# Kernel tuning notes

Hardware: AMD Instinct MI355X
Metric: run time of the kernel (lower is better)

Reference implementation:

```python
import jax, jax.numpy as jnp
import numpy as np

B, IN_DIM, UNITS = 16384, 3072, 3072  # batch, input_dim=3*unit1, units=3*unit2


def setup_inputs() -> dict:
    key = jax.random.key(0)
    k1, k2, k3 = jax.random.split(key, 3)
    inputs = jax.random.normal(k1, (B, IN_DIM), dtype=jnp.float32)
    # original init: uniform [0, 0.01) for w, zeros for b (gpe_bias = [0, 0])
    w = jax.random.uniform(k2, (IN_DIM, UNITS), dtype=jnp.float32, minval=0.0, maxval=0.01)
    b = jnp.zeros((UNITS,), dtype=jnp.float32)
    # per-unit binary diagonal mask, stored as [units, input_dim]
    mask = jax.random.randint(k3, (UNITS, IN_DIM), 0, 2, dtype=jnp.int32)
    return {"inputs": inputs, "w": w, "b": b, "mask": mask}


def reference(inputs, w, b, mask):
    # Original: p = transpose(s @ inputs^T, [2,0,1]) -> [batch, units, input_dim]
    #           f = diag_part(p @ w) + b            -> [batch, units]
    # Since s[u] = diag(mask[u]), this is exactly:
    #   f[b,u] = sum_i inputs[b,i] * mask[u,i] * w[i,u] + b[u]
    # i.e. a single masked GEMM with effective weight w * mask^T.
    w_eff = w * mask.T.astype(w.dtype)  # [input_dim, units]
    return inputs @ w_eff + b
```

## Files before the change

kernel.cpp:

```cpp
#include <hip/hip_runtime.h>

#define BATCH 16384
#define KDIM  3072
#define NDIM  3072

typedef __bf16 bf16;
typedef bf16  bf16x8  __attribute__((ext_vector_type(8)));
typedef float f32x4   __attribute__((ext_vector_type(4)));

__device__ __forceinline__ void g2l16(const bf16* g, bf16* l) {
    __builtin_amdgcn_global_load_lds(
        (__attribute__((address_space(1))) unsigned int*)g,
        (__attribute__((address_space(3))) unsigned int*)l,
        16, 0, 0);
}

__global__ __launch_bounds__(256) void cvt_a_kernel(const float* __restrict__ in,
                                                    bf16* __restrict__ out) {
    const long idx = (long)blockIdx.x * 256 + threadIdx.x;
    const float4* in4 = (const float4*)in;
    float4 a = in4[idx * 2];
    float4 b = in4[idx * 2 + 1];
    bf16x8 o;
    o[0] = (bf16)a.x; o[1] = (bf16)a.y; o[2] = (bf16)a.z; o[3] = (bf16)a.w;
    o[4] = (bf16)b.x; o[5] = (bf16)b.y; o[6] = (bf16)b.z; o[7] = (bf16)b.w;
    ((bf16x8*)out)[idx] = o;
}

__global__ __launch_bounds__(256) void weff_kernel(const float* __restrict__ w,
                                                   const int* __restrict__ mask,
                                                   bf16* __restrict__ wt) {
    __shared__ float tile[32][33];
    const int i0 = blockIdx.x * 32;
    const int u0 = blockIdx.y * 32;
    const int tx = threadIdx.x, ty = threadIdx.y;
#pragma unroll
    for (int r = 0; r < 4; r++)
        tile[ty + 8 * r][tx] = w[(long)(i0 + ty + 8 * r) * NDIM + u0 + tx];
    __syncthreads();
#pragma unroll
    for (int r = 0; r < 4; r++) {
        int u = u0 + ty + 8 * r;
        int i = i0 + tx;
        float v = tile[tx][ty + 8 * r] * (float)mask[(long)u * KDIM + i];
        wt[(long)u * KDIM + i] = (bf16)v;
    }
}

__global__ __launch_bounds__(512, 2) void gemm_kernel(const bf16* __restrict__ A,
                                                      const bf16* __restrict__ Bt,
                                                      const float* __restrict__ bias,
                                                      float* __restrict__ C) {
    __shared__ __align__(16) bf16 lds[2 * 32768];

    const int tid  = threadIdx.x;
    const int lane = tid & 63;
    const int wv   = tid >> 6;
    const int l15  = lane & 15;
    const int l4   = lane >> 4;
    const int sx   = l15 & 7;
    const int wm   = (wv >> 2) * 64;
    const int wn   = (wv & 3) * 32;

    const int lid = blockIdx.y * gridDim.x + blockIdx.x;
    const int sid = (lid & 7) * 96 + (lid >> 3);
    const long m0 = (long)(sid / 12) * 256;
    const long n0 = (long)(sid % 12) * 256;

    const int srow = tid >> 3;
    const int gsc  = (tid & 7) ^ (srow & 7);
    const bf16* gAb = A  + (m0 + srow) * (long)KDIM + gsc * 8;
    const bf16* gBb = Bt + (n0 + srow) * (long)KDIM + gsc * 8;

#define STAGE_A(Q, KT, H) do {                                                  \
    const bf16* g_ = gAb + (long)((H) * 128) * KDIM + (long)(KT) * 64;          \
    bf16* d_ = &lds[(Q) * 32768 + (H) * 8192 + tid * 8];                        \
    g2l16(g_, d_);                                                              \
    g2l16(g_ + (long)64 * KDIM, d_ + 4096);                                     \
} while (0)
#define STAGE_B(Q, KT, H) do {                                                  \
    const bf16* g_ = gBb + (long)((H) * 128) * KDIM + (long)(KT) * 64;          \
    bf16* d_ = &lds[(Q) * 32768 + 16384 + (H) * 8192 + tid * 8];                \
    g2l16(g_, d_);                                                              \
    g2l16(g_ + (long)64 * KDIM, d_ + 4096);                                     \
} while (0)

    const int aRow = (wm + l15) * 64;
    const int bRow = (wn + l15) * 64;
    const int cc0  = (l4 ^ sx) * 8;
    const int cc1  = cc0 ^ 32;

    bf16x8 aF[4][2];
    bf16x8 bF[4][2];
    f32x4  acc[8][4] = {};

#define RDA(BP, MH)                                                             \
    _Pragma("unroll") for (int f_ = 0; f_ < 4; ++f_) {                          \
        aF[f_][0] = *(const bf16x8*)((BP) + (MH) * 8192 + aRow + f_ * 1024 + cc0); \
        aF[f_][1] = *(const bf16x8*)((BP) + (MH) * 8192 + aRow + f_ * 1024 + cc1); \
    }
#define RDB(BP, NH)                                                             \
    _Pragma("unroll") for (int n_ = 0; n_ < 2; ++n_) {                          \
        bF[(NH) * 2 + n_][0] = *(const bf16x8*)((BP) + 16384 + (NH) * 8192 + bRow + n_ * 1024 + cc0); \
        bF[(NH) * 2 + n_][1] = *(const bf16x8*)((BP) + 16384 + (NH) * 8192 + bRow + n_ * 1024 + cc1); \
    }
#define MMQ(MH, NH)                                                             \
    _Pragma("unroll") for (int ks_ = 0; ks_ < 2; ++ks_)                         \
    _Pragma("unroll") for (int f_ = 0; f_ < 4; ++f_)                            \
    _Pragma("unroll") for (int n_ = 0; n_ < 2; ++n_)                            \
        acc[(MH) * 4 + f_][(NH) * 2 + n_] = __builtin_amdgcn_mfma_f32_16x16x32_bf16( \
            aF[f_][ks_], bF[(NH) * 2 + n_][ks_], acc[(MH) * 4 + f_][(NH) * 2 + n_], 0, 0, 0)

#define PHASE(P, MH, NH, READS, STAGE_STMT, DOVM) do {                          \
    const bf16* bp_ = &lds[(P) * 32768];                                        \
    READS;                                                                      \
    STAGE_STMT;                                                                 \
    __builtin_amdgcn_s_setprio(1);                                              \
    MMQ(MH, NH);                                                                \
    __builtin_amdgcn_s_setprio(0);                                              \
    __builtin_amdgcn_sched_barrier(0);                                          \
    if (DOVM) asm volatile("s_waitcnt vmcnt(4)" ::: "memory");                  \
    asm volatile("" ::: "memory");                                              \
    __builtin_amdgcn_s_barrier();                                               \
    asm volatile("" ::: "memory");                                              \
} while (0)

#define RD_AB(MH, NH) RDB(bp_, NH); RDA(bp_, MH)
#define RD_ONLYB(NH)  RDB(bp_, NH)
#define RD_ONLYA(MH)  RDA(bp_, MH)
#define RD_NONE       ((void)0)

    STAGE_A(0, 0, 0);
    STAGE_B(0, 0, 0);
    STAGE_B(0, 0, 1);
    STAGE_A(0, 0, 1);
    STAGE_A(1, 1, 0);
    STAGE_B(1, 1, 0);
    asm volatile("s_waitcnt vmcnt(4)" ::: "memory");
    __builtin_amdgcn_s_barrier();
    asm volatile("" ::: "memory");

    const int NT = KDIM / 64;
#pragma unroll 1
    for (int t = 0; t < NT; t += 2) {
        const int k1 = t + 1;
        const int k2 = (t + 2 < NT) ? t + 2 : 0;
        const int k3 = (t + 3 < NT) ? t + 3 : t + 3 - NT;
        PHASE(0, 0, 0, RD_AB(0, 0),  STAGE_B(1, k1, 1), 0);
        PHASE(0, 0, 1, RD_ONLYB(1),  STAGE_A(1, k1, 1), 0);
        PHASE(0, 1, 0, RD_ONLYA(1),  STAGE_A(0, k2, 0), 0);
        PHASE(0, 1, 1, RD_NONE,      STAGE_B(0, k2, 0), 1);
        PHASE(1, 0, 0, RD_AB(0, 0),  STAGE_B(0, k2, 1), 0);
        PHASE(1, 0, 1, RD_ONLYB(1),  STAGE_A(0, k2, 1), 0);
        PHASE(1, 1, 0, RD_ONLYA(1),  STAGE_A(1, k3, 0), 0);
        PHASE(1, 1, 1, RD_NONE,      STAGE_B(1, k3, 0), 1);
    }
    asm volatile("s_waitcnt vmcnt(0)" ::: "memory");

    float bv[4];
#pragma unroll
    for (int n_ = 0; n_ < 4; ++n_) {
        const long gc = n0 + ((n_ < 2) ? (wn + n_ * 16) : (128 + wn + (n_ - 2) * 16)) + l15;
        bv[n_] = bias[gc];
    }
#pragma unroll
    for (int f_ = 0; f_ < 8; ++f_) {
        const long gm = m0 + ((f_ < 4) ? (wm + f_ * 16) : (128 + wm + (f_ - 4) * 16)) + l4 * 4;
#pragma unroll
        for (int n_ = 0; n_ < 4; ++n_) {
            const long gc = n0 + ((n_ < 2) ? (wn + n_ * 16) : (128 + wn + (n_ - 2) * 16)) + l15;
#pragma unroll
            for (int r_ = 0; r_ < 4; ++r_)
                C[(gm + r_) * NDIM + gc] = acc[f_][n_][r_] + bv[n_];
        }
    }
#undef STAGE_A
#undef STAGE_B
#undef RDA
#undef RDB
#undef MMQ
#undef PHASE
#undef RD_AB
#undef RD_ONLYB
#undef RD_ONLYA
#undef RD_NONE
}

__global__ __launch_bounds__(256) void naive_kernel(const float* __restrict__ x,
                                                    const float* __restrict__ w,
                                                    const float* __restrict__ bias,
                                                    const int* __restrict__ mask,
                                                    float* __restrict__ out) {
    const long idx = (long)blockIdx.x * 256 + threadIdx.x;
    const long bi = idx / NDIM;
    const int u = (int)(idx % NDIM);
    float s = 0.f;
    for (int k = 0; k < KDIM; k++)
        s += x[bi * KDIM + k] * w[(long)k * NDIM + u] * (float)mask[(long)u * KDIM + k];
    out[idx] = s + bias[u];
}

extern "C" void kernel_launch(void* const* d_in, const int* in_sizes, int n_in,
                              void* d_out, int out_size, void* d_ws, size_t ws_size,
                              hipStream_t stream) {
    const float* x    = (const float*)d_in[0];
    const float* w    = (const float*)d_in[1];
    const float* bias = (const float*)d_in[2];
    const int*   mask = (const int*)d_in[3];
    float* out = (float*)d_out;

    const size_t needA = (size_t)BATCH * KDIM * sizeof(bf16);
    const size_t needW = (size_t)NDIM * KDIM * sizeof(bf16);

    if (ws_size < needA + needW) {
        const long total = (long)BATCH * NDIM;
        naive_kernel<<<(int)(total / 256), 256, 0, stream>>>(x, w, bias, mask, out);
        return;
    }

    bf16* Abf = (bf16*)d_ws;
    bf16* Wt  = (bf16*)((char*)d_ws + needA);

    cvt_a_kernel<<<(BATCH * (KDIM / 8)) / 256, 256, 0, stream>>>(x, Abf);
    weff_kernel<<<dim3(KDIM / 32, NDIM / 32), dim3(32, 8), 0, stream>>>(w, mask, Wt);
    gemm_kernel<<<dim3(NDIM / 256, BATCH / 256), 512, 0, stream>>>(Abf, Wt, bias, out);
}
```

Before: 610.4 us.

## Reschedule GEMM main loop to prefetch next tile's LDS fragments during MFMA

Restructures the eight-phase software pipeline of the bf16 MFMA GEMM. LDS fragment reads for the next sub-tile are now issued after the current MFMA group rather than before it, and the first fragments of the next buffer are read at the end of each tile, so LDS latency is hidden behind matrix math. Global-to-LDS staging is regrouped so that two stages are issued per phase. This raises register pressure from holding extra live fragments, and the ordering of barriers against buffer reuse needs care to stay correct.

```diff
diff --git a/kernel.cpp b/kernel.cpp
--- a/kernel.cpp
+++ b/kernel.cpp
@@ -111,49 +111,59 @@
         acc[(MH) * 4 + f_][(NH) * 2 + n_] = __builtin_amdgcn_mfma_f32_16x16x32_bf16( \
             aF[f_][ks_], bF[(NH) * 2 + n_][ks_], acc[(MH) * 4 + f_][(NH) * 2 + n_], 0, 0, 0)
 
-#define PHASE(P, MH, NH, READS, STAGE_STMT, DOVM) do {                          \
+#define PRIO1 __builtin_amdgcn_s_setprio(1)
+#define PRIO0 __builtin_amdgcn_s_setprio(0)
+#define SB    __builtin_amdgcn_sched_barrier(0)
+#define BAR   do { asm volatile("" ::: "memory"); __builtin_amdgcn_s_barrier(); \
+                   asm volatile("" ::: "memory"); } while (0)
+#define VM4   asm volatile("s_waitcnt vmcnt(4)" ::: "memory")
+
+#define TILE_BODY(P, K1, K2) do {                                               \
     const bf16* bp_ = &lds[(P) * 32768];                                        \
-    READS;                                                                      \
-    STAGE_STMT;                                                                 \
-    __builtin_amdgcn_s_setprio(1);                                              \
-    MMQ(MH, NH);                                                                \
-    __builtin_amdgcn_s_setprio(0);                                              \
-    __builtin_amdgcn_sched_barrier(0);                                          \
-    if (DOVM) asm volatile("s_waitcnt vmcnt(4)" ::: "memory");                  \
-    asm volatile("" ::: "memory");                                              \
-    __builtin_amdgcn_s_barrier();                                               \
-    asm volatile("" ::: "memory");                                              \
+    const bf16* bq_ = &lds[((P) ^ 1) * 32768];                                  \
+                              \
+    RDB(bp_, 1);                                                                \
+    STAGE_A((P) ^ 1, K1, 1);                                                    \
+    PRIO1; MMQ(0, 0); PRIO0;                                                    \
+    SB; BAR;                                                                    \
+       \
+    STAGE_B((P) ^ 1, K1, 1);                                                    \
+    PRIO1; MMQ(0, 1); PRIO0;                                                    \
+    RDA(bp_, 1);                                                                \
+    SB; BAR;                                                                    \
+                   \
+    STAGE_A(P, K2, 0);                                                          \
+    STAGE_B(P, K2, 0);                                                          \
+    PRIO1; MMQ(1, 0); PRIO0;                                                    \
+    SB; VM4; BAR;                                                               \
+            \
+    PRIO1; MMQ(1, 1); PRIO0;                                                    \
+    RDA(bq_, 0);                                                                \
+    RDB(bq_, 0);                                                                \
+    SB; BAR;                                                                    \
 } while (0)
-
-#define RD_AB(MH, NH) RDB(bp_, NH); RDA(bp_, MH)
-#define RD_ONLYB(NH)  RDB(bp_, NH)
-#define RD_ONLYA(MH)  RDA(bp_, MH)
-#define RD_NONE       ((void)0)
 
     STAGE_A(0, 0, 0);
     STAGE_B(0, 0, 0);
+    STAGE_A(0, 0, 1);
     STAGE_B(0, 0, 1);
-    STAGE_A(0, 0, 1);
     STAGE_A(1, 1, 0);
     STAGE_B(1, 1, 0);
     asm volatile("s_waitcnt vmcnt(4)" ::: "memory");
     __builtin_amdgcn_s_barrier();
     asm volatile("" ::: "memory");
+    RDA(&lds[0], 0);
+    RDB(&lds[0], 0);
 
     const int NT = KDIM / 64;
 #pragma unroll 1
     for (int t = 0; t < NT; t += 2) {
-        const int k1 = t + 1;
-        const int k2 = (t + 2 < NT) ? t + 2 : 0;
-        const int k3 = (t + 3 < NT) ? t + 3 : t + 3 - NT;
-        PHASE(0, 0, 0, RD_AB(0, 0),  STAGE_B(1, k1, 1), 0);
-        PHASE(0, 0, 1, RD_ONLYB(1),  STAGE_A(1, k1, 1), 0);
-        PHASE(0, 1, 0, RD_ONLYA(1),  STAGE_A(0, k2, 0), 0);
-        PHASE(0, 1, 1, RD_NONE,      STAGE_B(0, k2, 0), 1);
-        PHASE(1, 0, 0, RD_AB(0, 0),  STAGE_B(0, k2, 1), 0);
-        PHASE(1, 0, 1, RD_ONLYB(1),  STAGE_A(0, k2, 1), 0);
-        PHASE(1, 1, 0, RD_ONLYA(1),  STAGE_A(1, k3, 0), 0);
-        PHASE(1, 1, 1, RD_NONE,      STAGE_B(1, k3, 0), 1);
+        const int k1a = t + 1;
+        const int k2a = (t + 2 < NT) ? t + 2 : 0;
+        const int k1b = (t + 2 < NT) ? t + 2 : 0;
+        const int k2b = (t + 3 < NT) ? t + 3 : 0;
+        TILE_BODY(0, k1a, k2a);
+        TILE_BODY(1, k1b, k2b);
     }
     asm volatile("s_waitcnt vmcnt(0)" ::: "memory");
 
@@ -179,11 +189,12 @@
 #undef RDA
 #undef RDB
 #undef MMQ
-#undef PHASE
-#undef RD_AB
-#undef RD_ONLYB
-#undef RD_ONLYA
-#undef RD_NONE
+#undef TILE_BODY
+#undef PRIO1
+#undef PRIO0
+#undef SB
+#undef BAR
+#undef VM4
 }
 
 __global__ __launch_bounds__(256) void naive_kernel(const float* __restrict__ x,
```

After: 608.9 us. Within noise of the previous version (-0.3%).
